# Kernel tuning notes

Hardware: AMD Instinct MI355X
Metric: run time of the kernel (lower is better)

The kernel has to match this reference:

```python
import jax, jax.numpy as jnp
import numpy as np

N, E, H, K = 50000, 300000, 128, 50
PI = float(np.pi)
EPS = 1e-5


def gaussian_expand(ea, k):
    # RBF expansion of each edge feature into k gaussians on [0, 1]
    centers = jnp.linspace(0.0, 1.0, k)            # (k,)
    width = 1.0 / k
    g = jnp.exp(-((ea[..., None] - centers) ** 2) / (2.0 * width * width))  # (E, 4, k)
    return g.reshape(ea.shape[0], -1)              # (E, 4k)


def bn_train(z, g, b):
    # BatchNorm1d in training mode: biased batch stats
    m = jnp.mean(z, axis=0)
    v = jnp.mean(z * z, axis=0) - m * m
    return (z - m) * jax.lax.rsqrt(v + EPS) * g + b


def lrelu(z):
    return jnp.where(z >= 0, z, 0.01 * z)


def setup_inputs() -> dict:
    key = jax.random.key(0)
    ks = jax.random.split(key, 16)
    s = 0.02
    d = {
        "x": jax.random.normal(ks[0], (N, H), jnp.float32),
        "edge_attr": jax.random.uniform(ks[1], (E, 4), jnp.float32),
        "edge_index": jax.random.randint(ks[2], (2, E), 0, N, jnp.int32),
        # f_b: Linear(4K -> H)
        "Wb": jax.random.normal(ks[3], (4 * K, H), jnp.float32) * s,
        "bb": jnp.zeros((H,), jnp.float32),
        # f_e: Linear(3H->H) + LReLU + BN + Linear(H->H) + LReLU + BN + Linear(H->H)
        "We1": jax.random.normal(ks[4], (3 * H, H), jnp.float32) * s,
        "be1": jnp.zeros((H,), jnp.float32),
        "ge1": jnp.ones((H,), jnp.float32),
        "bte1": jnp.zeros((H,), jnp.float32),
        "We2": jax.random.normal(ks[5], (H, H), jnp.float32) * s,
        "be2": jnp.zeros((H,), jnp.float32),
        "ge2": jnp.ones((H,), jnp.float32),
        "bte2": jnp.zeros((H,), jnp.float32),
        "We3": jax.random.normal(ks[6], (H, H), jnp.float32) * s,
        "be3": jnp.zeros((H,), jnp.float32),
        # f_d: Linear(H->H)
        "Wd": jax.random.normal(ks[7], (H, H), jnp.float32) * s,
        "bd": jnp.zeros((H,), jnp.float32),
        # v parameter (1, H)
        "v": jnp.ones((1, H), jnp.float32),
        # f_n: Linear(H->H) + LReLU + BN + Linear(H->H)
        "Wn1": jax.random.normal(ks[8], (H, H), jnp.float32) * s,
        "bn1": jnp.zeros((H,), jnp.float32),
        "gn": jnp.ones((H,), jnp.float32),
        "btn": jnp.zeros((H,), jnp.float32),
        "Wn2": jax.random.normal(ks[9], (H, H), jnp.float32) * s,
        "bn2": jnp.zeros((H,), jnp.float32),
    }
    return d


def reference(x, edge_attr, edge_index, Wb, bb, We1, be1, ge1, bte1, We2, be2,
              ge2, bte2, We3, be3, Wd, bd, v, Wn1, bn1, gn, btn, Wn2, bn2):
    src, dst = edge_index[0], edge_index[1]
    gt = gaussian_expand(edge_attr, K) @ Wb + bb            # (E, H)
    coeff = jnp.cos(PI / 2 * edge_attr[:, 3])[:, None]      # (E, 1)
    h = jnp.concatenate([x[src], gt, x[dst]], axis=1)       # (E, 3H)
    h = bn_train(lrelu(h @ We1 + be1), ge1, bte1)
    h = bn_train(lrelu(h @ We2 + be2), ge2, bte2)
    cond_filter = coeff * (h @ We3 + be3)                   # (E, H)
    m_st = cond_filter * (x[src] @ Wd + bd)                 # (E, H)
    m_t = v * (x @ Wd + bd)                                 # (N, H)
    incoming = jax.ops.segment_sum(m_st, dst, num_segments=N)  # scatter_add + zero pad
    z = m_t + incoming
    out = bn_train(lrelu(z @ Wn1 + bn1), gn, btn) @ Wn2 + bn2 + x
    return out
```

## Files before the change

### kernel.cpp

```cpp
#include <hip/hip_runtime.h>

typedef __attribute__((ext_vector_type(8))) short bf16x8;
typedef __attribute__((ext_vector_type(4))) float f32x4;

#define DEVFN __device__ __forceinline__

DEVFN short f2bf(float f) {
    union { float f; unsigned u; } v; v.f = f;
    unsigned r = (v.u + 0x7FFFu + ((v.u >> 16) & 1u)) >> 16;
    return (short)(unsigned short)r;
}
DEVFN float bf2f(short h) {
    union { unsigned u; float f; } v; v.u = ((unsigned)(unsigned short)h) << 16;
    return v.f;
}
DEVFN unsigned packbf(float a, float b) {
    return (unsigned)(unsigned short)f2bf(a) | ((unsigned)(unsigned short)f2bf(b) << 16);
}

#define GLD_LDS16(gp, lp)                                                     \
    __builtin_amdgcn_global_load_lds(                                         \
        (const __attribute__((address_space(1))) unsigned*)(gp),              \
        (__attribute__((address_space(3))) unsigned*)(lp), 16, 0, 0)



__global__ __launch_bounds__(128) void build_w1p_k(
    const float* __restrict__ Wb, const float* __restrict__ We1,
    const float* __restrict__ bb, const float* __restrict__ be1,
    float* __restrict__ W1p, float* __restrict__ b1p)
{
    int j = threadIdx.x;
    const float* B = We1 + 128 * 128;
    int i = blockIdx.x;
    if (i < 200) {
        float a = 0.f;
        for (int m = 0; m < 128; m++) a += Wb[i * 128 + m] * B[m * 128 + j];
        W1p[i * 128 + j] = a;
    } else {
        float a = be1[j];
        for (int m = 0; m < 128; m++) a += bb[m] * B[m * 128 + j];
        b1p[j] = a;
    }
}

__global__ __launch_bounds__(128) void build_tab_k(
    const float* __restrict__ W1p, const float* __restrict__ b1p,
    short* __restrict__ tab)
{
    int i = blockIdx.x;
    int c = blockIdx.y;
    int j = threadIdx.x;
    float t = (float)i * (1.0f / 1024.0f);
    float acc = (c == 0) ? b1p[j] : 0.f;
    int kc = (int)(t * 49.f + 0.5f);
    for (int dk = -6; dk <= 6; dk++) {
        int k = kc + dk;
        if (k >= 0 && k < 50) {
            float d = t - (float)k * (1.f / 49.f);
            float g = expf(-1250.f * d * d);
            acc += g * W1p[(c * 50 + k) * 128 + j];
        }
    }
    tab[((size_t)(c * 1025 + i)) * 128 + j] = f2bf(acc);
}

__global__ __launch_bounds__(256) void fold_plain_k(
    const float* __restrict__ W0, const float* __restrict__ W1,
    const float* __restrict__ W2, const float* __restrict__ W3,
    short* __restrict__ O0, short* __restrict__ O1,
    short* __restrict__ O2, short* __restrict__ O3)
{
    const float* W = (blockIdx.y == 0) ? W0 : (blockIdx.y == 1) ? W1 : (blockIdx.y == 2) ? W2 : W3;
    short* O = (blockIdx.y == 0) ? O0 : (blockIdx.y == 1) ? O1 : (blockIdx.y == 2) ? O2 : O3;
    int idx = blockIdx.x * 256 + threadIdx.x;
    int n = idx >> 8, ks = (idx >> 6) & 3, lane = idx & 63;
    int k8 = ks * 32 + (lane >> 4) * 8;
    int pcol = (lane & 15) * 8 + n;
    bf16x8 fv;
    #pragma unroll
    for (int i2 = 0; i2 < 8; i2++) fv[i2] = f2bf(W[(k8 + i2) * 128 + pcol]);
    *(bf16x8*)(O + (size_t)idx * 8) = fv;
}

__global__ __launch_bounds__(256) void fold_k(
    const float* __restrict__ W, const float* __restrict__ bias,
    const float* __restrict__ statsG, const float* __restrict__ gamma,
    const float* __restrict__ beta, float invNs,
    short* __restrict__ Bp, float* __restrict__ biasOut)
{
    __shared__ float sS[128], sT[128];
    int tid = threadIdx.x;
    if (tid < 128) {
        float sum = 0.f, sq = 0.f;
        for (int r = 0; r < 16; r++) {
            sum += statsG[r * 256 + tid];
            sq  += statsG[r * 256 + 128 + tid];
        }
        float m = sum * invNs;
        float var = sq * invNs - m * m;
        float rs = rsqrtf(var + 1e-5f);
        float s = rs * gamma[tid];
        float t = beta[tid] - m * s;
        sS[tid] = s; sT[tid] = t;
    }
    __syncthreads();
    if (blockIdx.x == 0 && tid < 128) {
        float b = bias[tid];
        for (int k = 0; k < 128; k++) b += sT[k] * W[k * 128 + tid];
        biasOut[tid] = b;
    }
    int idx = blockIdx.x * 256 + tid;
    int n = idx >> 8, ks = (idx >> 6) & 3, lane = idx & 63;
    int k8 = ks * 32 + (lane >> 4) * 8;
    int pcol = (lane & 15) * 8 + n;
    bf16x8 fv;
    #pragma unroll
    for (int i2 = 0; i2 < 8; i2++)
        fv[i2] = f2bf(sS[k8 + i2] * W[(k8 + i2) * 128 + pcol]);
    *(bf16x8*)(Bp + (size_t)idx * 8) = fv;
}


__global__ __launch_bounds__(256) void hist_k(
    const int* __restrict__ dstI, int* __restrict__ cnt, int E)
{
    int e = blockIdx.x * 256 + threadIdx.x;
    if (e < E) atomicAdd(&cnt[dstI[e]], 1);
}

__global__ __launch_bounds__(256) void scan1_k(
    const int* __restrict__ cnt, int Nn, int* __restrict__ posE, int* __restrict__ bsum)
{
    __shared__ int s[256];
    int t = threadIdx.x, g = blockIdx.x * 256 + t;
    int v = (g < Nn) ? cnt[g] : 0;
    s[t] = v;
    __syncthreads();
    for (int off = 1; off < 256; off <<= 1) {
        int u = (t >= off) ? s[t - off] : 0;
        __syncthreads();
        s[t] += u;
        __syncthreads();
    }
    if (g < Nn) posE[g] = s[t] - v;
    if (t == 255) bsum[blockIdx.x] = s[255];
}

__global__ __launch_bounds__(256) void scan2_k(int* __restrict__ bsum, int nb)
{
    __shared__ int s[256];
    int t = threadIdx.x;
    int v = (t < nb) ? bsum[t] : 0;
    s[t] = v;
    __syncthreads();
    for (int off = 1; off < 256; off <<= 1) {
        int u = (t >= off) ? s[t - off] : 0;
        __syncthreads();
        s[t] += u;
        __syncthreads();
    }
    if (t < nb) bsum[t] = s[t] - v;
}

__global__ __launch_bounds__(256) void fix_k(
    const int* __restrict__ posE, const int* __restrict__ bsum,
    int* __restrict__ pos2, int Nn)
{
    int id = blockIdx.x * 256 + threadIdx.x;
    if (id < Nn) pos2[id] = posE[id] + bsum[id >> 8];
}

__global__ __launch_bounds__(256) void scat_k(
    const int* __restrict__ srcI, const int* __restrict__ dstI,
    const float4* __restrict__ ea4, int* __restrict__ pos2,
    int* __restrict__ sSrc, int* __restrict__ sDst,
    float* __restrict__ scf, float4* __restrict__ sEa, int E)
{
    int e = blockIdx.x * 256 + threadIdx.x;
    if (e >= E) return;
    int d = dstI[e];
    int p = atomicAdd(&pos2[d], 1);
    sSrc[p] = srcI[e];
    sDst[p] = d;
    float4 ev = ea4[e];
    sEa[p] = ev;
    scf[p] = cosf(1.57079632679f * ev.w);
}

__global__ __launch_bounds__(256, 4) void node_all_k(
    const float* __restrict__ x, int M,
    const short* __restrict__ bp3,
    const float* __restrict__ bd, const float* __restrict__ vv,
    short* __restrict__ xd, short* __restrict__ zaccb,
    short* __restrict__ xs1b, short* __restrict__ xt1b)
{
    int tid = threadIdx.x;
    int wave = tid >> 6, lane = tid & 63;
    int kgrp = lane >> 4, colbase = lane & 15;
    int chunk = blockIdx.x;
    int rowA = chunk * 64 + wave * 16 + colbase;
    bool rv = rowA < M;

    bf16x8 af[4];
    #pragma unroll
    for (int ks = 0; ks < 4; ks++) {
        bf16x8 v = (bf16x8){0,0,0,0,0,0,0,0};
        if (rv) {
            const float* ap = x + (size_t)rowA * 128 + ks * 32 + kgrp * 8;
            float4 f0 = ((const float4*)ap)[0];
            float4 f1 = ((const float4*)ap)[1];
            v[0] = f2bf(f0.x); v[1] = f2bf(f0.y); v[2] = f2bf(f0.z); v[3] = f2bf(f0.w);
            v[4] = f2bf(f1.x); v[5] = f2bf(f1.y); v[6] = f2bf(f1.z); v[7] = f2bf(f1.w);
        }
        af[ks] = v;
    }

    float bcol[8], vcol[8];
    *(float4*)&bcol[0] = *(const float4*)(bd + colbase * 8);
    *(float4*)&bcol[4] = *(const float4*)(bd + colbase * 8 + 4);
    *(float4*)&vcol[0] = *(const float4*)(vv + colbase * 8);
    *(float4*)&vcol[4] = *(const float4*)(vv + colbase * 8 + 4);

    int rbase = chunk * 64 + wave * 16 + kgrp * 4;

    for (int b = 0; b < 3; b++) {
        const short* Bb = bp3 + (size_t)b * 16384;
        f32x4 acc[8];
        #pragma unroll
        for (int n = 0; n < 8; n++) acc[n] = (f32x4){0.f, 0.f, 0.f, 0.f};
        #pragma unroll
        for (int ks = 0; ks < 4; ks++) {
            #pragma unroll
            for (int n = 0; n < 8; n++) {
                bf16x8 bf = *(const bf16x8*)(Bb + ((size_t)((n * 4 + ks) * 64 + lane)) * 8);
                acc[n] = __builtin_amdgcn_mfma_f32_16x16x32_bf16(af[ks], bf, acc[n], 0, 0, 0);
            }
        }
        if (b == 0) {
            #pragma unroll
            for (int r = 0; r < 4; r++) {
                int row = rbase + r;
                if (row < M) {
                    bf16x8 xo, zo;
                    #pragma unroll
                    for (int n = 0; n < 8; n++) {
                        float val = acc[n][r] + bcol[n];
                        xo[n] = f2bf(val);
                        zo[n] = f2bf(vcol[n] * val);
                    }
                    *(bf16x8*)(xd    + (size_t)row * 128 + colbase * 8) = xo;
                    *(bf16x8*)(zaccb + (size_t)row * 128 + colbase * 8) = zo;
                }
            }
        } else {
            short* outp = (b == 1) ? xs1b : xt1b;
            #pragma unroll
            for (int r = 0; r < 4; r++) {
                int row = rbase + r;
                if (row < M) {
                    bf16x8 o;
                    #pragma unroll
                    for (int n = 0; n < 8; n++) o[n] = f2bf(acc[n][r]);
                    *(bf16x8*)(outp + (size_t)row * 128 + colbase * 8) = o;
                }
            }
        }
    }
}

__global__ __launch_bounds__(256) void edge_z1_k(
    const short* __restrict__ xs1b, const short* __restrict__ xt1b,
    const short* __restrict__ tab,
    const int* __restrict__ sSrc, const int* __restrict__ sDst,
    const float4* __restrict__ sEa,
    short* __restrict__ z1, float* __restrict__ stats, int Etot)
{
    int tid = threadIdx.x, wave = tid >> 6, lane = tid & 63;
    int colg = lane & 15, esub = lane >> 4;
    int e0 = blockIdx.x * 256 + wave * 64;

    int eL = e0 + lane;
    int myS = 0, myD = 0;
    float4 myE = {0.f, 0.f, 0.f, 0.f};
    if (eL < Etot) { myS = sSrc[eL]; myD = sDst[eL]; myE = sEa[eL]; }

    float sacc[8], qacc[8];
    #pragma unroll
    for (int j = 0; j < 8; j++) { sacc[j] = 0.f; qacc[j] = 0.f; }

    int ni = Etot - e0; if (ni > 64) ni = 64;
    int nsteps = (ni + 3) >> 2;

    for (int st = 0; st < nsteps; st++) {
        int i = st * 4 + esub;
        bool valid = i < ni;
        int s = __shfl(myS, i);
        int d = __shfl(myD, i);
        float tv[4];
        tv[0] = __shfl(myE.x, i); tv[1] = __shfl(myE.y, i);
        tv[2] = __shfl(myE.z, i); tv[3] = __shfl(myE.w, i);

        bf16x8 xs8 = *(const bf16x8*)(xs1b + (size_t)s * 128 + colg * 8);
        bf16x8 xt8 = *(const bf16x8*)(xt1b + (size_t)d * 128 + colg * 8);

        float p[8];
        #pragma unroll
        for (int j = 0; j < 8; j++) p[j] = bf2f(xs8[j]) + bf2f(xt8[j]);

        #pragma unroll
        for (int c = 0; c < 4; c++) {
            float u = tv[c] * 1024.f;
            int i0 = (int)u;
            if (i0 > 1023) i0 = 1023;
            if (i0 < 0) i0 = 0;
            float f = u - (float)i0;
            const short* tb = tab + ((size_t)(c * 1025 + i0)) * 128 + colg * 8;
            bf16x8 t0 = *(const bf16x8*)tb;
            bf16x8 t1 = *(const bf16x8*)(tb + 128);
            #pragma unroll
            for (int j = 0; j < 8; j++) {
                float v0 = bf2f(t0[j]);
                p[j] += v0 + f * (bf2f(t1[j]) - v0);
            }
        }

        bf16x8 o;
        #pragma unroll
        for (int j = 0; j < 8; j++) {
            float z = p[j] >= 0.f ? p[j] : 0.01f * p[j];
            o[j] = f2bf(z);
            if (valid) { sacc[j] += z; qacc[j] += z * z; }
        }
        if (valid)
            *(bf16x8*)(z1 + (size_t)(e0 + i) * 128 + colg * 8) = o;
    }

    __shared__ float lS[128], lQ[128];
    if (tid < 128) { lS[tid] = 0.f; lQ[tid] = 0.f; }
    __syncthreads();
    #pragma unroll
    for (int j = 0; j < 8; j++) {
        atomicAdd(&lS[colg * 8 + j], sacc[j]);
        atomicAdd(&lQ[colg * 8 + j], qacc[j]);
    }
    __syncthreads();
    if (tid < 128) {
        int rep = blockIdx.x & 15;
        atomicAdd(&stats[rep * 256 + tid], lS[tid]);
        atomicAdd(&stats[rep * 256 + 128 + tid], lQ[tid]);
    }
}

__global__ __launch_bounds__(256) void segred_k(
    const short* __restrict__ cond, const short* __restrict__ xd,
    const int* __restrict__ sSrc, const int* __restrict__ endPos,
    short* __restrict__ zaccb, int Nn)
{
    int tid = threadIdx.x, wave = tid >> 6, lane = tid & 63;
    int colg = lane & 7;
    int esub = lane >> 3;
    int d0 = blockIdx.x * 64 + wave * 16;

    for (int i = 0; i < 16; i++) {
        int d = d0 + i;
        if (d >= Nn) break;
        int s0 = (d == 0) ? 0 : endPos[d - 1];
        int s1 = endPos[d];
        if (s1 <= s0) continue;

        float acc[16];
        #pragma unroll
        for (int j = 0; j < 16; j++) acc[j] = 0.f;

        for (int t = s0 + esub; t < s1; t += 8) {
            const short* cp = cond + (size_t)t * 128 + colg * 16;
            bf16x8 c0 = *(const bf16x8*)cp;
            bf16x8 c1 = *(const bf16x8*)(cp + 8);
            int s = sSrc[t];
            const short* xp = xd + (size_t)s * 128 + colg * 16;
            bf16x8 x0 = *(const bf16x8*)xp;
            bf16x8 x1 = *(const bf16x8*)(xp + 8);
            #pragma unroll
            for (int j = 0; j < 8; j++) {
                acc[j]     += bf2f(c0[j]) * bf2f(x0[j]);
                acc[8 + j] += bf2f(c1[j]) * bf2f(x1[j]);
            }
        }

        #pragma unroll
        for (int j = 0; j < 16; j++) {
            acc[j] += __shfl_xor(acc[j], 8);
            acc[j] += __shfl_xor(acc[j], 16);
            acc[j] += __shfl_xor(acc[j], 32);
        }

        if (esub == 0) {
            short* zp = zaccb + (size_t)d * 128 + colg * 16;
            bf16x8 z0 = *(const bf16x8*)zp;
            bf16x8 z1 = *(const bf16x8*)(zp + 8);
            bf16x8 o0, o1;
            #pragma unroll
            for (int j = 0; j < 8; j++) {
                o0[j] = f2bf(bf2f(z0[j]) + acc[j]);
                o1[j] = f2bf(bf2f(z1[j]) + acc[8 + j]);
            }
            *(bf16x8*)zp = o0;
            *(bf16x8*)(zp + 8) = o1;
        }
    }
}

template<int EPI>
__global__ __launch_bounds__(256, 2) void pgemm_k(
    const short* __restrict__ A, int M,
    const short* __restrict__ Bp, const float* __restrict__ bias,
    void* __restrict__ out, float* __restrict__ stats,
    const short* __restrict__ xd, short* __restrict__ zaccb,
    const float* __restrict__ scf, const int* __restrict__ sSrc,
    const int* __restrict__ sDst, const float* __restrict__ xres)
{
    __shared__ __align__(16) short ldsB[16384];
    __shared__ float lS[128], lQ[128];
    int tid = threadIdx.x;
    int wave = tid >> 6, lane = tid & 63;
    int kgrp = lane >> 4, colbase = lane & 15;

    #pragma unroll
    for (int i = 0; i < 8; i++) {
        int off = (i * 256 + wave * 64 + lane) * 8;
        GLD_LDS16(Bp + off, ldsB + off);
    }

    int c0 = blockIdx.x * 4;
    bf16x8 af[4][4];
    #pragma unroll
    for (int j = 0; j < 4; j++) {
        int rowA = (c0 + j) * 64 + wave * 16 + colbase;
        bool rv = rowA < M;
        #pragma unroll
        for (int ks = 0; ks < 4; ks++)
            af[j][ks] = rv ? *(const bf16x8*)(A + (size_t)rowA * 128 + ks * 32 + kgrp * 8)
                           : (bf16x8){0,0,0,0,0,0,0,0};
    }

    float bcol[8];
    *(float4*)&bcol[0] = *(const float4*)(bias + colbase * 8);
    *(float4*)&bcol[4] = *(const float4*)(bias + colbase * 8 + 4);

    float sreg[8], qreg[8];
    if (EPI == 2) {
        #pragma unroll
        for (int n = 0; n < 8; n++) { sreg[n] = 0.f; qreg[n] = 0.f; }
        if (tid < 128) { lS[tid] = 0.f; lQ[tid] = 0.f; }
    }

    __syncthreads();

    #pragma unroll
    for (int j = 0; j < 4; j++) {
        int chunk = c0 + j;
        if (chunk * 64 >= M) break;
        int rbase = chunk * 64 + wave * 16 + kgrp * 4;

        float mcf[4];
        if (EPI == 3) {
            #pragma unroll
            for (int r = 0; r < 4; r++) {
                int row = rbase + r;
                mcf[r] = (row < M) ? scf[row] : 0.f;
            }
        }

        f32x4 acc[8];
        #pragma unroll
        for (int n = 0; n < 8; n++) acc[n] = (f32x4){0.f, 0.f, 0.f, 0.f};
        #pragma unroll
        for (int ks = 0; ks < 4; ks++) {
            #pragma unroll
            for (int n = 0; n < 8; n++) {
                bf16x8 bf = *(const bf16x8*)(ldsB + ((size_t)((n * 4 + ks) * 64 + lane)) * 8);
                acc[n] = __builtin_amdgcn_mfma_f32_16x16x32_bf16(af[j][ks], bf, acc[n], 0, 0, 0);
            }
        }

        if (EPI == 2) {
            short* outh = (short*)out;
            #pragma unroll
            for (int r = 0; r < 4; r++) {
                int row = rbase + r;
                bf16x8 o;
                #pragma unroll
                for (int n = 0; n < 8; n++) {
                    float z = acc[n][r] + bcol[n];
                    z = z >= 0.f ? z : 0.01f * z;
                    if (row >= M) z = 0.f;
                    sreg[n] += z; qreg[n] += z * z;
                    o[n] = f2bf(z);
                }
                if (row < M)
                    *(bf16x8*)(outh + (size_t)row * 128 + colbase * 8) = o;
            }
        } else if (EPI == 3) {
            short* outh = (short*)out;
            #pragma unroll
            for (int r = 0; r < 4; r++) {
                int row = rbase + r;
                if (row < M) {
                    bf16x8 o;
                    #pragma unroll
                    for (int n = 0; n < 8; n++)
                        o[n] = f2bf(mcf[r] * (acc[n][r] + bcol[n]));
                    *(bf16x8*)(outh + (size_t)row * 128 + colbase * 8) = o;
                }
            }
        } else if (EPI == 4) {
            float* outf = (float*)out;
            #pragma unroll
            for (int r = 0; r < 4; r++) {
                int row = rbase + r;
                if (row < M) {
                    const float4* xr = (const float4*)(xres + (size_t)row * 128 + colbase * 8);
                    float4 x0 = xr[0], x1 = xr[1];
                    float4 o0, o1;
                    o0.x = acc[0][r] + bcol[0] + x0.x;
                    o0.y = acc[1][r] + bcol[1] + x0.y;
                    o0.z = acc[2][r] + bcol[2] + x0.z;
                    o0.w = acc[3][r] + bcol[3] + x0.w;
                    o1.x = acc[4][r] + bcol[4] + x1.x;
                    o1.y = acc[5][r] + bcol[5] + x1.y;
                    o1.z = acc[6][r] + bcol[6] + x1.z;
                    o1.w = acc[7][r] + bcol[7] + x1.w;
                    float4* op = (float4*)(outf + (size_t)row * 128 + colbase * 8);
                    op[0] = o0; op[1] = o1;
                }
            }
        }
    }

    if (EPI == 2) {
        __syncthreads();
        #pragma unroll
        for (int n = 0; n < 8; n++) {
            atomicAdd(&lS[colbase * 8 + n], sreg[n]);
            atomicAdd(&lQ[colbase * 8 + n], qreg[n]);
        }
        __syncthreads();
        if (tid < 128) {
            int rep = blockIdx.x & 15;
            atomicAdd(&stats[rep * 256 + tid], lS[tid]);
            atomicAdd(&stats[rep * 256 + 128 + tid], lQ[tid]);
        }
    }
}

extern "C" void kernel_launch(void* const* d_in, const int* in_sizes, int n_in,
                              void* d_out, int out_size, void* d_ws, size_t ws_size,
                              hipStream_t stream)
{
    const float* x    = (const float*)d_in[0];
    const float* ea   = (const float*)d_in[1];
    const int*   eidx = (const int*)d_in[2];
    const float* Wb   = (const float*)d_in[3];
    const float* bb   = (const float*)d_in[4];
    const float* We1  = (const float*)d_in[5];
    const float* be1  = (const float*)d_in[6];
    const float* ge1  = (const float*)d_in[7];
    const float* bte1 = (const float*)d_in[8];
    const float* We2  = (const float*)d_in[9];
    const float* be2  = (const float*)d_in[10];
    const float* ge2  = (const float*)d_in[11];
    const float* bte2 = (const float*)d_in[12];
    const float* We3  = (const float*)d_in[13];
    const float* be3  = (const float*)d_in[14];
    const float* Wd   = (const float*)d_in[15];
    const float* bd   = (const float*)d_in[16];
    const float* vv   = (const float*)d_in[17];
    const float* Wn1  = (const float*)d_in[18];
    const float* bn1  = (const float*)d_in[19];
    const float* gn   = (const float*)d_in[20];
    const float* btn  = (const float*)d_in[21];
    const float* Wn2  = (const float*)d_in[22];
    const float* bn2  = (const float*)d_in[23];

    const int NN = in_sizes[0] / 128;
    const int EE = in_sizes[1] / 4;

    char* ws = (char*)d_ws;
    size_t oEZ   = 0;
    size_t oXD   = oEZ   + (size_t)EE * 256;
    size_t oXS   = oXD   + (size_t)NN * 256;
    size_t oXT   = oXS   + (size_t)NN * 256;
    size_t oZACC = oXT   + (size_t)NN * 256;
    size_t oZN   = oZACC + (size_t)NN * 256;
    size_t oTAB  = oZN   + (size_t)NN * 256;
    size_t oW1P  = oTAB  + (size_t)4 * 1025 * 256;
    size_t oB1P  = oW1P  + (size_t)200 * 512;
    size_t oBP   = oB1P  + 512;
    size_t oBIAS = oBP   + (size_t)7 * 32768;
    size_t oST   = oBIAS + (size_t)7 * 512;
    size_t oCNT  = oST   + 49152;
    size_t oPOS  = oCNT  + 201728;
    size_t oBSUM = oPOS  + 201728;
    size_t oPOS2 = oBSUM + 1024;
    size_t oSSRC = oPOS2 + 201728;
    size_t oSDST = oSSRC + (size_t)EE * 4;
    size_t oSCF  = oSDST + (size_t)EE * 4;
    size_t oSEA  = (oSCF + (size_t)EE * 4 + 15) & ~(size_t)15;

    short* eZ    = (short*)(ws + oEZ);
    short* xd    = (short*)(ws + oXD);
    short* xs1b  = (short*)(ws + oXS);
    short* xt1b  = (short*)(ws + oXT);
    short* zaccb = (short*)(ws + oZACC);
    short* zn    = (short*)(ws + oZN);
    short* tab   = (short*)(ws + oTAB);
    float* W1p   = (float*)(ws + oW1P);
    float* b1p   = (float*)(ws + oB1P);
    short* bp    = (short*)(ws + oBP);
    short* BpW2  = bp + 3 * 16384;
    short* BpW3  = bp + 4 * 16384;
    short* BpN1  = bp + 5 * 16384;
    short* BpN2  = bp + 6 * 16384;
    float* bo    = (float*)(ws + oBIAS);
    float* b2p   = bo + 0 * 128;
    float* b3p   = bo + 1 * 128;
    float* b2np  = bo + 2 * 128;
    float* st1   = (float*)(ws + oST);
    float* st2   = st1 + 4096;
    float* stN   = st1 + 8192;
    int*   cnt   = (int*)(ws + oCNT);
    int*   posE  = (int*)(ws + oPOS);
    int*   bsum  = (int*)(ws + oBSUM);
    int*   pos2  = (int*)(ws + oPOS2);
    int*   sSrc  = (int*)(ws + oSSRC);
    int*   sDst  = (int*)(ws + oSDST);
    float* scf   = (float*)(ws + oSCF);
    float4* sEa  = (float4*)(ws + oSEA);

    hipMemsetAsync(ws + oST, 0, 49152 + 201728, stream);

    build_w1p_k<<<201, 128, 0, stream>>>(Wb, We1, bb, be1, W1p, b1p);
    build_tab_k<<<dim3(1025, 4), 128, 0, stream>>>(W1p, b1p, tab);
    fold_plain_k<<<dim3(8, 4), 256, 0, stream>>>(
        Wd, We1, We1 + 256 * 128, Wn1, bp, bp + 16384, bp + 2 * 16384, BpN1);

    int nchN = (NN + 63) / 64;
    int nchE = (EE + 63) / 64;
    int gN4 = (nchN + 3) / 4;
    int gE4 = (nchE + 3) / 4;
    int nbN = (NN + 255) / 256;
    int nbE = (EE + 255) / 256;
    int nbSeg = (NN + 63) / 64;

    node_all_k<<<nchN, 256, 0, stream>>>(x, NN, bp, bd, vv, xd, zaccb, xs1b, xt1b);

    hist_k<<<nbE, 256, 0, stream>>>(eidx + EE, cnt, EE);
    scan1_k<<<nbN, 256, 0, stream>>>(cnt, NN, posE, bsum);
    scan2_k<<<1, 256, 0, stream>>>(bsum, nbN);
    fix_k<<<nbN, 256, 0, stream>>>(posE, bsum, pos2, NN);
    scat_k<<<nbE, 256, 0, stream>>>(eidx, eidx + EE, (const float4*)ea, pos2,
                                    sSrc, sDst, scf, sEa, EE);

    edge_z1_k<<<nbE, 256, 0, stream>>>(xs1b, xt1b, tab, sSrc, sDst, sEa, eZ, st1, EE);

    fold_k<<<8, 256, 0, stream>>>(We2, be2, st1, ge1, bte1, 1.f / (float)EE, BpW2, b2p);
    pgemm_k<2><<<gE4, 256, 0, stream>>>(eZ, EE, BpW2, b2p, eZ, st2,
        nullptr, nullptr, nullptr, nullptr, nullptr, nullptr);

    fold_k<<<8, 256, 0, stream>>>(We3, be3, st2, ge2, bte2, 1.f / (float)EE, BpW3, b3p);
    pgemm_k<3><<<gE4, 256, 0, stream>>>(eZ, EE, BpW3, b3p, eZ, nullptr,
        nullptr, nullptr, scf, nullptr, nullptr, nullptr);

    segred_k<<<nbSeg, 256, 0, stream>>>(eZ, xd, sSrc, pos2, zaccb, NN);

    pgemm_k<2><<<gN4, 256, 0, stream>>>(zaccb, NN, BpN1, bn1, zn, stN,
        nullptr, nullptr, nullptr, nullptr, nullptr, nullptr);

    fold_k<<<8, 256, 0, stream>>>(Wn2, bn2, stN, gn, btn, 1.f / (float)NN, BpN2, b2np);
    pgemm_k<4><<<gN4, 256, 0, stream>>>(zn, NN, BpN2, b2np, d_out, nullptr,
        nullptr, nullptr, nullptr, nullptr, nullptr, x);
}
```

Before: 450.0 us.

## Make pgemm a persistent grid-stride kernel that prefetches the next A tile

The pgemm kernel no longer preloads four fixed 64-row chunks per block. It now loops over chunks with a grid stride and loads the next chunk's A fragments into registers while it computes the current one. The edge GEMM grids are capped at 1024 blocks and the node GEMM grids at 512 blocks. Each block's LDS weight load then covers a variable number of chunks, A-fragment register use drops, and global loads overlap MFMA work. The node GEMMs also get more blocks than before, in exchange for a runtime loop and register double-buffering.

```diff
diff --git a/kernel.cpp b/kernel.cpp
--- a/kernel.cpp
+++ b/kernel.cpp
@@ -432,16 +432,17 @@
         GLD_LDS16(Bp + off, ldsB + off);
     }
 
-    int c0 = blockIdx.x * 4;
-    bf16x8 af[4][4];
-    #pragma unroll
-    for (int j = 0; j < 4; j++) {
-        int rowA = (c0 + j) * 64 + wave * 16 + colbase;
-        bool rv = rowA < M;
+    int nch = (M + 63) >> 6;
+    int c = blockIdx.x;
+
+    bf16x8 afc[4];
+    {
+        int rowA = c * 64 + wave * 16 + colbase;
+        bool rv = (c < nch) && (rowA < M);
         #pragma unroll
         for (int ks = 0; ks < 4; ks++)
-            af[j][ks] = rv ? *(const bf16x8*)(A + (size_t)rowA * 128 + ks * 32 + kgrp * 8)
-                           : (bf16x8){0,0,0,0,0,0,0,0};
+            afc[ks] = rv ? *(const bf16x8*)(A + (size_t)rowA * 128 + ks * 32 + kgrp * 8)
+                         : (bf16x8){0,0,0,0,0,0,0,0};
     }
 
     float bcol[8];
@@ -457,11 +458,19 @@
 
     __syncthreads();
 
-    #pragma unroll
-    for (int j = 0; j < 4; j++) {
-        int chunk = c0 + j;
-        if (chunk * 64 >= M) break;
-        int rbase = chunk * 64 + wave * 16 + kgrp * 4;
+    for (; c < nch; c += gridDim.x) {
+        int cn = c + gridDim.x;
+        bf16x8 afn[4];
+        {
+            int rowA = cn * 64 + wave * 16 + colbase;
+            bool rv = (cn < nch) && (rowA < M);
+            #pragma unroll
+            for (int ks = 0; ks < 4; ks++)
+                afn[ks] = rv ? *(const bf16x8*)(A + (size_t)rowA * 128 + ks * 32 + kgrp * 8)
+                             : (bf16x8){0,0,0,0,0,0,0,0};
+        }
+
+        int rbase = c * 64 + wave * 16 + kgrp * 4;
 
         float mcf[4];
         if (EPI == 3) {
@@ -480,7 +489,7 @@
             #pragma unroll
             for (int n = 0; n < 8; n++) {
                 bf16x8 bf = *(const bf16x8*)(ldsB + ((size_t)((n * 4 + ks) * 64 + lane)) * 8);
-                acc[n] = __builtin_amdgcn_mfma_f32_16x16x32_bf16(af[j][ks], bf, acc[n], 0, 0, 0);
+                acc[n] = __builtin_amdgcn_mfma_f32_16x16x32_bf16(afc[ks], bf, acc[n], 0, 0, 0);
             }
         }
 
@@ -536,6 +545,9 @@
                 }
             }
         }
+
+        #pragma unroll
+        for (int ks = 0; ks < 4; ks++) afc[ks] = afn[ks];
     }
 
     if (EPI == 2) {
@@ -647,11 +659,12 @@
 
     int nchN = (NN + 63) / 64;
     int nchE = (EE + 63) / 64;
-    int gN4 = (nchN + 3) / 4;
-    int gE4 = (nchE + 3) / 4;
     int nbN = (NN + 255) / 256;
     int nbE = (EE + 255) / 256;
     int nbSeg = (NN + 63) / 64;
+
+    int gridE = nchE < 1024 ? nchE : 1024;
+    int gridN = nchN < 512 ? nchN : 512;
 
     node_all_k<<<nchN, 256, 0, stream>>>(x, NN, bp, bd, vv, xd, zaccb, xs1b, xt1b);
 
@@ -665,19 +678,19 @@
     edge_z1_k<<<nbE, 256, 0, stream>>>(xs1b, xt1b, tab, sSrc, sDst, sEa, eZ, st1, EE);
 
     fold_k<<<8, 256, 0, stream>>>(We2, be2, st1, ge1, bte1, 1.f / (float)EE, BpW2, b2p);
-    pgemm_k<2><<<gE4, 256, 0, stream>>>(eZ, EE, BpW2, b2p, eZ, st2,
+    pgemm_k<2><<<gridE, 256, 0, stream>>>(eZ, EE, BpW2, b2p, eZ, st2,
         nullptr, nullptr, nullptr, nullptr, nullptr, nullptr);
 
     fold_k<<<8, 256, 0, stream>>>(We3, be3, st2, ge2, bte2, 1.f / (float)EE, BpW3, b3p);
-    pgemm_k<3><<<gE4, 256, 0, stream>>>(eZ, EE, BpW3, b3p, eZ, nullptr,
+    pgemm_k<3><<<gridE, 256, 0, stream>>>(eZ, EE, BpW3, b3p, eZ, nullptr,
         nullptr, nullptr, scf, nullptr, nullptr, nullptr);
 
     segred_k<<<nbSeg, 256, 0, stream>>>(eZ, xd, sSrc, pos2, zaccb, NN);
 
-    pgemm_k<2><<<gN4, 256, 0, stream>>>(zaccb, NN, BpN1, bn1, zn, stN,
+    pgemm_k<2><<<gridN, 256, 0, stream>>>(zaccb, NN, BpN1, bn1, zn, stN,
         nullptr, nullptr, nullptr, nullptr, nullptr, nullptr);
 
     fold_k<<<8, 256, 0, stream>>>(Wn2, bn2, stN, gn, btn, 1.f / (float)NN, BpN2, b2np);
-    pgemm_k<4><<<gN4, 256, 0, stream>>>(zn, NN, BpN2, b2np, d_out, nullptr,
+    pgemm_k<4><<<gridN, 256, 0, stream>>>(zn, NN, BpN2, b2np, d_out, nullptr,
         nullptr, nullptr, nullptr, nullptr, nullptr, x);
 }
```

New measurement: 437.3 us. 1.03x faster.
